# Kernel optimization log

Hardware: AMD Instinct MI355X
Metric: run time of the kernel (lower is better)

Reference implementation:

```python
import jax, jax.numpy as jnp
import numpy as np

B, D, F, FH = 8, 16, 16, 128
L = D * D
EPS = 1e-5


def _coords():
    i = np.arange(L, dtype=np.float64)
    c0 = ((i + 1) / D - D / 2) / (D / 2)
    c1 = ((i + 1) % D - D / 2) / (D / 2)
    return jnp.asarray(np.stack([c0, c1], axis=1), dtype=jnp.float32)  # (L, 2)


def setup_inputs() -> dict:
    key = jax.random.key(0)
    ks = jax.random.split(key, 16)
    s = 0.05
    fin = F + 2
    inp = {
        "x": jax.random.normal(ks[0], (B, F, D, D), jnp.float32),
        # g_fc1 weight split into the x_i half (first f+2 cols) and x_j half
        "W1a": jax.random.normal(ks[1], (fin, FH), jnp.float32) * s,
        "W1b": jax.random.normal(ks[2], (fin, FH), jnp.float32) * s,
        "b1": jnp.zeros((FH,), jnp.float32),
        "g1_gamma": jnp.ones((FH,), jnp.float32), "g1_beta": jnp.zeros((FH,), jnp.float32),
        "W2": jax.random.normal(ks[3], (FH, FH), jnp.float32) * s, "b2": jnp.zeros((FH,), jnp.float32),
        "g2_gamma": jnp.ones((FH,), jnp.float32), "g2_beta": jnp.zeros((FH,), jnp.float32),
        "W3": jax.random.normal(ks[4], (FH, FH), jnp.float32) * s, "b3": jnp.zeros((FH,), jnp.float32),
        "g3_gamma": jnp.ones((FH,), jnp.float32), "g3_beta": jnp.zeros((FH,), jnp.float32),
        "Wagg": jax.random.normal(ks[5], (L,), jnp.float32) * s, "bagg": jnp.zeros((), jnp.float32),
        "Wf": jax.random.normal(ks[6], (FH, FH), jnp.float32) * s, "bf": jnp.zeros((FH,), jnp.float32),
        "f_gamma": jnp.ones((FH,), jnp.float32), "f_beta": jnp.zeros((FH,), jnp.float32),
        "Wo2": jax.random.normal(ks[7], (FH, FH), jnp.float32) * s, "bo2": jnp.zeros((FH,), jnp.float32),
        "o2_gamma": jnp.ones((FH,), jnp.float32), "o2_beta": jnp.zeros((FH,), jnp.float32),
        "Wo3": jax.random.normal(ks[8], (FH, F), jnp.float32) * s, "bo3": jnp.zeros((F,), jnp.float32),
        "coord": _coords(),
    }
    return inp


def _bn(h, gamma, beta):
    # torch BatchNorm1d (training mode) applied over channel dim = last axis here;
    # stats over (batch, length), biased variance.
    mu = jnp.mean(h, axis=(0, 1))
    var = jnp.mean((h - mu) ** 2, axis=(0, 1))
    return gamma * (h - mu) * jax.lax.rsqrt(var + EPS) + beta


def reference(x, W1a, W1b, b1, g1_gamma, g1_beta, W2, b2, g2_gamma, g2_beta,
              W3, b3, g3_gamma, g3_beta, Wagg, bagg, Wf, bf, f_gamma, f_beta,
              Wo2, bo2, o2_gamma, o2_beta, Wo3, bo3, coord):
    b, f, d = x.shape[0], x.shape[1], x.shape[2]
    l = d * d
    x_flat = x.reshape(b, f, l).transpose(0, 2, 1)                     # (b, L, f)
    x_flat = jnp.concatenate([x_flat, jnp.broadcast_to(coord, (b, l, 2))], axis=2)  # (b, L, f+2)
    # g_fc1 on cat([x_i, x_j]): x_i varies along pair-dim2 (index l), x_j along dim1 (index k)
    hi = x_flat @ W1a                                                  # (b, L, FH)
    hj = x_flat @ W1b                                                  # (b, L, FH)
    h = hi[:, None, :, :] + hj[:, :, None, :] + b1                     # (b, L, L, FH)
    h = h.reshape(b, l * l, -1)
    h = jax.nn.relu(_bn(h, g1_gamma, g1_beta))
    h = jax.nn.relu(_bn(h @ W2 + b2, g2_gamma, g2_beta))
    h = jax.nn.relu(_bn(h @ W3 + b3, g3_gamma, g3_beta))
    x_g = h.reshape(b, l, l, -1)                                       # (b, k, l, FH)
    # affine_aggregate: Linear(L -> 1) over the l (dim2) axis after permute
    x_agg = jnp.einsum('bklf,l->bkf', x_g, Wagg) + bagg                # (b, L, FH)
    x_f = jax.nn.relu(_bn(x_agg @ Wf + bf, f_gamma, f_beta))
    xo = jax.nn.relu(_bn(x_f @ Wo2 + bo2, o2_gamma, o2_beta))
    out = xo @ Wo3 + bo3                                               # (b, L, f)
    return out.reshape(b, d, d, f).transpose(0, 3, 1, 2)               # (b, f, d, d)
```

## Files before the change

kernel.cpp:

```cpp
#include <hip/hip_runtime.h>
#include <hip/hip_bf16.h>

typedef __bf16 bf16x8 __attribute__((ext_vector_type(8)));
typedef float  f32x4  __attribute__((ext_vector_type(4)));

static constexpr size_t HI_OFF  = 0;
static constexpr size_t HJ_OFF  = HI_OFF + (1u << 20);
static constexpr size_t Z_OFF   = HJ_OFF + (1u << 20);
static constexpr size_t PS_OFF  = Z_OFF + (size_t)524288 * 128 * 2;
static constexpr size_t PQ_OFF  = PS_OFF + (size_t)4096 * 128 * 4;
static constexpr size_t S1I_OFF = PQ_OFF + (size_t)4096 * 128 * 4;
static constexpr size_t S2I_OFF = S1I_OFF + 4096;
static constexpr size_t S1J_OFF = S2I_OFF + 4096;
static constexpr size_t S2J_OFF = S1J_OFF + 4096;
static constexpr size_t A1_OFF  = S2J_OFF + 4096;
static constexpr size_t D1_OFF  = A1_OFF + 512;
static constexpr size_t A2_OFF  = D1_OFF + 512;
static constexpr size_t C2_OFF  = A2_OFF + 512;
static constexpr size_t A3_OFF  = C2_OFF + 512;
static constexpr size_t C3_OFF  = A3_OFF + 512;
static constexpr size_t AF_OFF  = C3_OFF + 512;
static constexpr size_t CF_OFF  = AF_OFF + 512;
static constexpr size_t AO_OFF  = CF_OFF + 512;
static constexpr size_t CO_OFF  = AO_OFF + 512;
static constexpr size_t W2T_OFF = CO_OFF + 512;
static constexpr size_t W3T_OFF = W2T_OFF + 32768;
static constexpr size_t XAGG_OFF = W3T_OFF + 32768;
static constexpr size_t Y1_OFF  = XAGG_OFF + (1u << 20);
static constexpr size_t Y2_OFF  = Y1_OFF + (1u << 20);
static constexpr size_t TPS_OFF = Y2_OFF + (1u << 20);
static constexpr size_t TPQ_OFF = TPS_OFF + 65536;

__global__ void build_h(const float* __restrict__ x, const float* __restrict__ coord,
                        const float* __restrict__ W1a, const float* __restrict__ W1b,
                        float* __restrict__ hi, float* __restrict__ hj)
{
    __shared__ float xr[18];
    int bl = blockIdx.x;
    int b = bl >> 8, l = bl & 255;
    int t = threadIdx.x;
    if (t < 18)
        xr[t] = (t < 16) ? x[((size_t)b * 16 + t) * 256 + l] : coord[l * 2 + (t - 16)];
    __syncthreads();
    float ai = 0.f, aj = 0.f;
#pragma unroll
    for (int c = 0; c < 18; ++c) {
        float xv = xr[c];
        ai += xv * W1a[c * 128 + t];
        aj += xv * W1b[c * 128 + t];
    }
    hi[(size_t)bl * 128 + t] = ai;
    hj[(size_t)bl * 128 + t] = aj;
}

__global__ void stats1(const float* __restrict__ hi, const float* __restrict__ hj,
                       float* __restrict__ S1i, float* __restrict__ S2i,
                       float* __restrict__ S1j, float* __restrict__ S2j)
{
    int b = blockIdx.x, f = threadIdx.x;
    float s1i = 0, s2i = 0, s1j = 0, s2j = 0;
    for (int l = 0; l < 256; ++l) {
        float vi = hi[((size_t)b * 256 + l) * 128 + f];
        float vj = hj[((size_t)b * 256 + l) * 128 + f];
        s1i += vi; s2i += vi * vi;
        s1j += vj; s2j += vj * vj;
    }
    S1i[b * 128 + f] = s1i; S2i[b * 128 + f] = s2i;
    S1j[b * 128 + f] = s1j; S2j[b * 128 + f] = s2j;
}

__global__ void bn1_finalize(const float* __restrict__ S1i, const float* __restrict__ S2i,
                             const float* __restrict__ S1j, const float* __restrict__ S2j,
                             const float* __restrict__ g, const float* __restrict__ be,
                             float* __restrict__ a1, float* __restrict__ d1,
                             const float* __restrict__ W2, const float* __restrict__ W3,
                             __bf16* __restrict__ W2t, __bf16* __restrict__ W3t)
{
    int f = threadIdx.x;
    float s1i = 0, s2i = 0, s1j = 0, s2j = 0;
    float mib[8], mjb[8];
#pragma unroll
    for (int b = 0; b < 8; ++b) {
        float x1 = S1i[b * 128 + f]; s1i += x1; mib[b] = x1 * (1.f / 256.f);
        s2i += S2i[b * 128 + f];
        float x2 = S1j[b * 128 + f]; s1j += x2; mjb[b] = x2 * (1.f / 256.f);
        s2j += S2j[b * 128 + f];
    }
    const float invN = 1.f / 2048.f;
    float mi = s1i * invN, mj = s1j * invN;
    float vu = s2i * invN - mi * mi;
    float vv = s2j * invN - mj * mj;
    float cr = 0.f;
#pragma unroll
    for (int b = 0; b < 8; ++b) cr += (mib[b] - mi) * (mjb[b] - mj);
    cr *= (1.f / 8.f);
    float var = vu + vv + 2.f * cr;
    float av = g[f] * rsqrtf(var + 1e-5f);
    a1[f] = av;
    d1[f] = be[f] - av * (mi + mj);
    for (int k = 0; k < 128; ++k) {
        W2t[f * 128 + k] = (__bf16)W2[k * 128 + f];
        W3t[f * 128 + k] = (__bf16)W3[k * 128 + f];
    }
}

__global__ __launch_bounds__(256) void pair_gemm1(
    const float* __restrict__ hi, const float* __restrict__ hj,
    const float* __restrict__ a1, const float* __restrict__ d1,
    const __bf16* __restrict__ W2t,
    __bf16* __restrict__ Z, float* __restrict__ ps, float* __restrict__ pq)
{
    __shared__ __align__(16) char hA[32768];
    __shared__ __align__(16) char wB[32768];
    __shared__ float red[1024];

    int blk = blockIdx.x;
    int half = blk & 1;
    int bk = blk >> 1;
    int b = bk >> 8;
    int t = threadIdx.x;
    int lane = t & 63;
    int wave = t >> 6;
    int fc = (t & 15) * 8;
    int rg = t >> 4;

    float a1v[8], qv[8];
    const float* hjrow = hj + (size_t)bk * 128 + fc;
    const float* d1p = d1 + fc;
    const float* a1p = a1 + fc;
#pragma unroll
    for (int j = 0; j < 8; ++j) { a1v[j] = a1p[j]; qv[j] = a1v[j] * hjrow[j] + d1p[j]; }

    const float* hib = hi + ((size_t)b * 256 + half * 128) * 128;
#pragma unroll
    for (int rr = 0; rr < 128; rr += 16) {
        int row = rr + rg;
        const float* src = hib + row * 128 + fc;
        bf16x8 v;
#pragma unroll
        for (int j = 0; j < 8; ++j) {
            float h = fmaxf(a1v[j] * src[j] + qv[j], 0.f);
            v[j] = (__bf16)h;
        }
        int byte = (row * 256 + fc * 2) ^ ((row & 7) << 4);
        *reinterpret_cast<bf16x8*>(hA + byte) = v;
        bf16x8 w = *reinterpret_cast<const bf16x8*>(W2t + row * 128 + fc);
        *reinterpret_cast<bf16x8*>(wB + byte) = w;
    }
    __syncthreads();

    f32x4 acc[2][8] = {};
    int arow0 = wave * 32 + (lane & 15);
    int kg = (lane >> 4) * 8;
#pragma unroll
    for (int kk = 0; kk < 128; kk += 32) {
        bf16x8 af[2], bfr[8];
#pragma unroll
        for (int m = 0; m < 2; ++m) {
            int row = arow0 + m * 16;
            int byte = (row * 256 + (kk + kg) * 2) ^ ((row & 7) << 4);
            af[m] = *reinterpret_cast<const bf16x8*>(hA + byte);
        }
#pragma unroll
        for (int n = 0; n < 8; ++n) {
            int col = n * 16 + (lane & 15);
            int byte = (col * 256 + (kk + kg) * 2) ^ ((col & 7) << 4);
            bfr[n] = *reinterpret_cast<const bf16x8*>(wB + byte);
        }
#pragma unroll
        for (int m = 0; m < 2; ++m)
#pragma unroll
            for (int n = 0; n < 8; ++n)
                acc[m][n] = __builtin_amdgcn_mfma_f32_16x16x32_bf16(af[m], bfr[n], acc[m][n], 0, 0, 0);
    }

    __bf16* zb = Z + ((size_t)bk * 256 + half * 128) * 128;
    float s[8] = {}, q[8] = {};
    int r0 = (lane >> 4) * 4;
    int cl = lane & 15;
#pragma unroll
    for (int m = 0; m < 2; ++m)
#pragma unroll
        for (int n = 0; n < 8; ++n)
#pragma unroll
            for (int r = 0; r < 4; ++r) {
                float v = acc[m][n][r];
                int row = wave * 32 + m * 16 + r0 + r;
                zb[row * 128 + n * 16 + cl] = (__bf16)v;
                s[n] += v; q[n] += v * v;
            }
#pragma unroll
    for (int n = 0; n < 8; ++n) {
        s[n] += __shfl_xor(s[n], 16); s[n] += __shfl_xor(s[n], 32);
        q[n] += __shfl_xor(q[n], 16); q[n] += __shfl_xor(q[n], 32);
    }
    if (lane < 16) {
#pragma unroll
        for (int n = 0; n < 8; ++n) {
            red[wave * 256 + n * 16 + cl] = s[n];
            red[wave * 256 + 128 + n * 16 + cl] = q[n];
        }
    }
    __syncthreads();
    {
        int f = t & 127, which = t >> 7;
        float a = red[0 * 256 + which * 128 + f] + red[1 * 256 + which * 128 + f]
                + red[2 * 256 + which * 128 + f] + red[3 * 256 + which * 128 + f];
        if (which == 0) ps[(size_t)blk * 128 + f] = a;
        else            pq[(size_t)blk * 128 + f] = a;
    }
}

__global__ __launch_bounds__(256) void pair_gemm2(
    __bf16* __restrict__ Z,
    const float* __restrict__ a2, const float* __restrict__ c2,
    const __bf16* __restrict__ W3t,
    float* __restrict__ ps, float* __restrict__ pq)
{
    __shared__ __align__(16) char hA[32768];
    __shared__ __align__(16) char wB[32768];
    __shared__ float red[1024];

    int blk = blockIdx.x;
    int half = blk & 1;
    int bk = blk >> 1;
    int t = threadIdx.x;
    int lane = t & 63;
    int wave = t >> 6;
    int fc = (t & 15) * 8;
    int rg = t >> 4;

    float a2v[8], c2v[8];
#pragma unroll
    for (int j = 0; j < 8; ++j) { a2v[j] = a2[fc + j]; c2v[j] = c2[fc + j]; }

    __bf16* zbase = Z + ((size_t)bk * 256 + half * 128) * 128;
#pragma unroll
    for (int rr = 0; rr < 128; rr += 16) {
        int row = rr + rg;
        bf16x8 zv = *reinterpret_cast<const bf16x8*>(zbase + row * 128 + fc);
        bf16x8 v;
#pragma unroll
        for (int j = 0; j < 8; ++j) {
            float h = fmaxf(a2v[j] * (float)zv[j] + c2v[j], 0.f);
            v[j] = (__bf16)h;
        }
        int byte = (row * 256 + fc * 2) ^ ((row & 7) << 4);
        *reinterpret_cast<bf16x8*>(hA + byte) = v;
        bf16x8 w = *reinterpret_cast<const bf16x8*>(W3t + row * 128 + fc);
        *reinterpret_cast<bf16x8*>(wB + byte) = w;
    }
    __syncthreads();

    f32x4 acc[2][8] = {};
    int arow0 = wave * 32 + (lane & 15);
    int kg = (lane >> 4) * 8;
#pragma unroll
    for (int kk = 0; kk < 128; kk += 32) {
        bf16x8 af[2], bfr[8];
#pragma unroll
        for (int m = 0; m < 2; ++m) {
            int row = arow0 + m * 16;
            int byte = (row * 256 + (kk + kg) * 2) ^ ((row & 7) << 4);
            af[m] = *reinterpret_cast<const bf16x8*>(hA + byte);
        }
#pragma unroll
        for (int n = 0; n < 8; ++n) {
            int col = n * 16 + (lane & 15);
            int byte = (col * 256 + (kk + kg) * 2) ^ ((col & 7) << 4);
            bfr[n] = *reinterpret_cast<const bf16x8*>(wB + byte);
        }
#pragma unroll
        for (int m = 0; m < 2; ++m)
#pragma unroll
            for (int n = 0; n < 8; ++n)
                acc[m][n] = __builtin_amdgcn_mfma_f32_16x16x32_bf16(af[m], bfr[n], acc[m][n], 0, 0, 0);
    }

    float s[8] = {}, q[8] = {};
    int r0 = (lane >> 4) * 4;
    int cl = lane & 15;
#pragma unroll
    for (int m = 0; m < 2; ++m)
#pragma unroll
        for (int n = 0; n < 8; ++n)
#pragma unroll
            for (int r = 0; r < 4; ++r) {
                float v = acc[m][n][r];
                int row = wave * 32 + m * 16 + r0 + r;
                zbase[row * 128 + n * 16 + cl] = (__bf16)v;
                s[n] += v; q[n] += v * v;
            }
#pragma unroll
    for (int n = 0; n < 8; ++n) {
        s[n] += __shfl_xor(s[n], 16); s[n] += __shfl_xor(s[n], 32);
        q[n] += __shfl_xor(q[n], 16); q[n] += __shfl_xor(q[n], 32);
    }
    if (lane < 16) {
#pragma unroll
        for (int n = 0; n < 8; ++n) {
            red[wave * 256 + n * 16 + cl] = s[n];
            red[wave * 256 + 128 + n * 16 + cl] = q[n];
        }
    }
    __syncthreads();
    {
        int f = t & 127, which = t >> 7;
        float a = red[0 * 256 + which * 128 + f] + red[1 * 256 + which * 128 + f]
                + red[2 * 256 + which * 128 + f] + red[3 * 256 + which * 128 + f];
        if (which == 0) ps[(size_t)blk * 128 + f] = a;
        else            pq[(size_t)blk * 128 + f] = a;
    }
}

__global__ void finalize_bn(const float* __restrict__ ps, const float* __restrict__ pq,
                            int nblk, float inv_count,
                            const float* __restrict__ gamma, const float* __restrict__ beta,
                            float* __restrict__ a, float* __restrict__ c)
{
    __shared__ float rs[256], rq[256];
    int f = blockIdx.x, t = threadIdx.x;
    float s = 0, q = 0;
    for (int i = t; i < nblk; i += 256) {
        s += ps[(size_t)i * 128 + f];
        q += pq[(size_t)i * 128 + f];
    }
    rs[t] = s; rq[t] = q;
    __syncthreads();
    for (int st = 128; st > 0; st >>= 1) {
        if (t < st) { rs[t] += rs[t + st]; rq[t] += rq[t + st]; }
        __syncthreads();
    }
    if (t == 0) {
        float mean = rs[0] * inv_count;
        float var = rq[0] * inv_count - mean * mean;
        float av = gamma[f] * rsqrtf(var + 1e-5f);
        a[f] = av;
        c[f] = beta[f] - av * mean;
    }
}

__global__ void aggregate(const __bf16* __restrict__ Z,
                          const float* __restrict__ a3, const float* __restrict__ c3,
                          const float* __restrict__ Wagg, const float* __restrict__ bagg,
                          float* __restrict__ xagg)
{
    int bk = blockIdx.x;
    int f = threadIdx.x;
    const __bf16* zb = Z + (size_t)bk * 256 * 128 + f;
    float av = a3[f], cv = c3[f];
    float acc = 0.f;
#pragma unroll 4
    for (int l = 0; l < 256; ++l) {
        float v = (float)zb[(size_t)l * 128];
        v = fmaxf(av * v + cv, 0.f);
        acc += v * Wagg[l];
    }
    xagg[(size_t)bk * 128 + f] = acc + bagg[0];
}

__global__ void tail_gemm(const float* __restrict__ X,
                          const float* __restrict__ aIn, const float* __restrict__ cIn, int relu_in,
                          const float* __restrict__ W, const float* __restrict__ bias,
                          float* __restrict__ Y, float* __restrict__ ps, float* __restrict__ pq)
{
    __shared__ float xs[2048];
    __shared__ float rsum[256];
    int blk = blockIdx.x, t = threadIdx.x;
    for (int i = t; i < 2048; i += 256) {
        float v = X[(size_t)blk * 2048 + i];
        if (relu_in) { int f = i & 127; v = fmaxf(aIn[f] * v + cIn[f], 0.f); }
        xs[i] = v;
    }
    __syncthreads();
    int col = t & 127, hf = t >> 7;
    float bv = bias[col];
    float acc[8];
#pragma unroll
    for (int r = 0; r < 8; ++r) acc[r] = bv;
    for (int k = 0; k < 128; ++k) {
        float w = W[k * 128 + col];
#pragma unroll
        for (int r = 0; r < 8; ++r) acc[r] += xs[(hf * 8 + r) * 128 + k] * w;
    }
    float s = 0, q = 0;
#pragma unroll
    for (int r = 0; r < 8; ++r) {
        Y[((size_t)blk * 16 + hf * 8 + r) * 128 + col] = acc[r];
        s += acc[r]; q += acc[r] * acc[r];
    }
    rsum[t] = s; __syncthreads();
    if (hf == 0) ps[(size_t)blk * 128 + col] = rsum[col] + rsum[128 + col];
    __syncthreads();
    rsum[t] = q; __syncthreads();
    if (hf == 0) pq[(size_t)blk * 128 + col] = rsum[col] + rsum[128 + col];
}

__global__ void tail_out(const float* __restrict__ Y2,
                         const float* __restrict__ ao, const float* __restrict__ co,
                         const float* __restrict__ Wo3, const float* __restrict__ bo3,
                         float* __restrict__ out)
{
    __shared__ float xs[2048];
    int blk = blockIdx.x, t = threadIdx.x;
    for (int i = t; i < 2048; i += 256) {
        int f = i & 127;
        xs[i] = fmaxf(ao[f] * Y2[(size_t)blk * 2048 + i] + co[f], 0.f);
    }
    __syncthreads();
    int col = t & 15, r = t >> 4;
    float acc = bo3[col];
    for (int k = 0; k < 128; ++k) acc += xs[r * 128 + k] * Wo3[k * 16 + col];
    int grow = blk * 16 + r;
    int b = grow >> 8, l = grow & 255;
    out[((size_t)b * 16 + col) * 256 + l] = acc;
}

extern "C" void kernel_launch(void* const* d_in, const int* in_sizes, int n_in,
                              void* d_out, int out_size, void* d_ws, size_t ws_size,
                              hipStream_t stream)
{
    const float* x     = (const float*)d_in[0];
    const float* W1a   = (const float*)d_in[1];
    const float* W1b   = (const float*)d_in[2];
    const float* g1g   = (const float*)d_in[4];
    const float* g1b   = (const float*)d_in[5];
    const float* W2    = (const float*)d_in[6];
    const float* g2g   = (const float*)d_in[8];
    const float* g2b   = (const float*)d_in[9];
    const float* W3    = (const float*)d_in[10];
    const float* g3g   = (const float*)d_in[12];
    const float* g3b   = (const float*)d_in[13];
    const float* Wagg  = (const float*)d_in[14];
    const float* bagg  = (const float*)d_in[15];
    const float* Wf    = (const float*)d_in[16];
    const float* bf_   = (const float*)d_in[17];
    const float* fg    = (const float*)d_in[18];
    const float* fb    = (const float*)d_in[19];
    const float* Wo2   = (const float*)d_in[20];
    const float* bo2   = (const float*)d_in[21];
    const float* og    = (const float*)d_in[22];
    const float* ob    = (const float*)d_in[23];
    const float* Wo3   = (const float*)d_in[24];
    const float* bo3   = (const float*)d_in[25];
    const float* coord = (const float*)d_in[26];

    char* ws = (char*)d_ws;
    float*  HI   = (float*)(ws + HI_OFF);
    float*  HJ   = (float*)(ws + HJ_OFF);
    __bf16* Z    = (__bf16*)(ws + Z_OFF);
    float*  PS   = (float*)(ws + PS_OFF);
    float*  PQ   = (float*)(ws + PQ_OFF);
    float*  S1I  = (float*)(ws + S1I_OFF);
    float*  S2I  = (float*)(ws + S2I_OFF);
    float*  S1J  = (float*)(ws + S1J_OFF);
    float*  S2J  = (float*)(ws + S2J_OFF);
    float*  A1   = (float*)(ws + A1_OFF);
    float*  D1   = (float*)(ws + D1_OFF);
    float*  A2   = (float*)(ws + A2_OFF);
    float*  C2   = (float*)(ws + C2_OFF);
    float*  A3   = (float*)(ws + A3_OFF);
    float*  C3   = (float*)(ws + C3_OFF);
    float*  AF   = (float*)(ws + AF_OFF);
    float*  CF   = (float*)(ws + CF_OFF);
    float*  AO   = (float*)(ws + AO_OFF);
    float*  CO   = (float*)(ws + CO_OFF);
    __bf16* W2T  = (__bf16*)(ws + W2T_OFF);
    __bf16* W3T  = (__bf16*)(ws + W3T_OFF);
    float*  XAGG = (float*)(ws + XAGG_OFF);
    float*  Y1   = (float*)(ws + Y1_OFF);
    float*  Y2   = (float*)(ws + Y2_OFF);
    float*  TPS  = (float*)(ws + TPS_OFF);
    float*  TPQ  = (float*)(ws + TPQ_OFF);

    build_h<<<2048, 128, 0, stream>>>(x, coord, W1a, W1b, HI, HJ);
    stats1<<<8, 128, 0, stream>>>(HI, HJ, S1I, S2I, S1J, S2J);
    bn1_finalize<<<1, 128, 0, stream>>>(S1I, S2I, S1J, S2J, g1g, g1b, A1, D1, W2, W3, W2T, W3T);

    pair_gemm1<<<4096, 256, 0, stream>>>(HI, HJ, A1, D1, W2T, Z, PS, PQ);
    finalize_bn<<<128, 256, 0, stream>>>(PS, PQ, 4096, 1.f / 524288.f, g2g, g2b, A2, C2);

    pair_gemm2<<<4096, 256, 0, stream>>>(Z, A2, C2, W3T, PS, PQ);
    finalize_bn<<<128, 256, 0, stream>>>(PS, PQ, 4096, 1.f / 524288.f, g3g, g3b, A3, C3);

    aggregate<<<2048, 128, 0, stream>>>(Z, A3, C3, Wagg, bagg, XAGG);

    tail_gemm<<<128, 256, 0, stream>>>(XAGG, A1, D1, 0, Wf, bf_, Y1, TPS, TPQ);
    finalize_bn<<<128, 256, 0, stream>>>(TPS, TPQ, 128, 1.f / 2048.f, fg, fb, AF, CF);

    tail_gemm<<<128, 256, 0, stream>>>(Y1, AF, CF, 1, Wo2, bo2, Y2, TPS, TPQ);
    finalize_bn<<<128, 256, 0, stream>>>(TPS, TPQ, 128, 1.f / 2048.f, og, ob, AO, CO);

    tail_out<<<128, 256, 0, stream>>>(Y2, AO, CO, Wo3, bo3, (float*)d_out);

    (void)in_sizes; (void)n_in; (void)out_size; (void)ws_size;
}
```

Baseline: 217.1 us.

## Recompute layer-3 GEMM fused with aggregation instead of writing Z back

```diff
diff --git a/kernel.cpp b/kernel.cpp
--- a/kernel.cpp
+++ b/kernel.cpp
@@ -2,18 +2,22 @@
 #include <hip/hip_bf16.h>
 
 typedef __bf16 bf16x8 __attribute__((ext_vector_type(8)));
+typedef __bf16 bf16x4 __attribute__((ext_vector_type(4)));
 typedef float  f32x4  __attribute__((ext_vector_type(4)));
 
+static constexpr size_t MB = 1u << 20;
 static constexpr size_t HI_OFF  = 0;
-static constexpr size_t HJ_OFF  = HI_OFF + (1u << 20);
-static constexpr size_t Z_OFF   = HJ_OFF + (1u << 20);
+static constexpr size_t HJ_OFF  = HI_OFF + MB;
+static constexpr size_t HIS_OFF = HJ_OFF + MB;
+static constexpr size_t QV_OFF  = HIS_OFF + MB;
+static constexpr size_t Z_OFF   = QV_OFF + MB;
 static constexpr size_t PS_OFF  = Z_OFF + (size_t)524288 * 128 * 2;
 static constexpr size_t PQ_OFF  = PS_OFF + (size_t)4096 * 128 * 4;
 static constexpr size_t S1I_OFF = PQ_OFF + (size_t)4096 * 128 * 4;
-static constexpr size_t S2I_OFF = S1I_OFF + 4096;
-static constexpr size_t S1J_OFF = S2I_OFF + 4096;
-static constexpr size_t S2J_OFF = S1J_OFF + 4096;
-static constexpr size_t A1_OFF  = S2J_OFF + 4096;
+static constexpr size_t S2I_OFF = S1I_OFF + 32768;
+static constexpr size_t S1J_OFF = S2I_OFF + 32768;
+static constexpr size_t S2J_OFF = S1J_OFF + 32768;
+static constexpr size_t A1_OFF  = S2J_OFF + 32768;
 static constexpr size_t D1_OFF  = A1_OFF + 512;
 static constexpr size_t A2_OFF  = D1_OFF + 512;
 static constexpr size_t C2_OFF  = A2_OFF + 512;
@@ -26,9 +30,9 @@
 static constexpr size_t W2T_OFF = CO_OFF + 512;
 static constexpr size_t W3T_OFF = W2T_OFF + 32768;
 static constexpr size_t XAGG_OFF = W3T_OFF + 32768;
-static constexpr size_t Y1_OFF  = XAGG_OFF + (1u << 20);
-static constexpr size_t Y2_OFF  = Y1_OFF + (1u << 20);
-static constexpr size_t TPS_OFF = Y2_OFF + (1u << 20);
+static constexpr size_t Y1_OFF  = XAGG_OFF + MB;
+static constexpr size_t Y2_OFF  = Y1_OFF + MB;
+static constexpr size_t TPS_OFF = Y2_OFF + MB;
 static constexpr size_t TPQ_OFF = TPS_OFF + 65536;
 
 __global__ void build_h(const float* __restrict__ x, const float* __restrict__ coord,
@@ -57,34 +61,41 @@
                        float* __restrict__ S1i, float* __restrict__ S2i,
                        float* __restrict__ S1j, float* __restrict__ S2j)
 {
-    int b = blockIdx.x, f = threadIdx.x;
+    int g = blockIdx.x;
+    int b = g >> 3, lg = g & 7;
+    int f = threadIdx.x;
     float s1i = 0, s2i = 0, s1j = 0, s2j = 0;
-    for (int l = 0; l < 256; ++l) {
+#pragma unroll 4
+    for (int i = 0; i < 32; ++i) {
+        int l = lg * 32 + i;
         float vi = hi[((size_t)b * 256 + l) * 128 + f];
         float vj = hj[((size_t)b * 256 + l) * 128 + f];
         s1i += vi; s2i += vi * vi;
         s1j += vj; s2j += vj * vj;
     }
-    S1i[b * 128 + f] = s1i; S2i[b * 128 + f] = s2i;
-    S1j[b * 128 + f] = s1j; S2j[b * 128 + f] = s2j;
+    S1i[g * 128 + f] = s1i; S2i[g * 128 + f] = s2i;
+    S1j[g * 128 + f] = s1j; S2j[g * 128 + f] = s2j;
 }
 
 __global__ void bn1_finalize(const float* __restrict__ S1i, const float* __restrict__ S2i,
                              const float* __restrict__ S1j, const float* __restrict__ S2j,
                              const float* __restrict__ g, const float* __restrict__ be,
-                             float* __restrict__ a1, float* __restrict__ d1,
-                             const float* __restrict__ W2, const float* __restrict__ W3,
-                             __bf16* __restrict__ W2t, __bf16* __restrict__ W3t)
+                             float* __restrict__ a1, float* __restrict__ d1)
 {
     int f = threadIdx.x;
     float s1i = 0, s2i = 0, s1j = 0, s2j = 0;
     float mib[8], mjb[8];
 #pragma unroll
     for (int b = 0; b < 8; ++b) {
-        float x1 = S1i[b * 128 + f]; s1i += x1; mib[b] = x1 * (1.f / 256.f);
-        s2i += S2i[b * 128 + f];
-        float x2 = S1j[b * 128 + f]; s1j += x2; mjb[b] = x2 * (1.f / 256.f);
-        s2j += S2j[b * 128 + f];
+        float sb = 0, sbj = 0;
+#pragma unroll
+        for (int lg = 0; lg < 8; ++lg) {
+            int gg = b * 8 + lg;
+            sb  += S1i[gg * 128 + f]; s2i += S2i[gg * 128 + f];
+            sbj += S1j[gg * 128 + f]; s2j += S2j[gg * 128 + f];
+        }
+        mib[b] = sb * (1.f / 256.f); mjb[b] = sbj * (1.f / 256.f);
+        s1i += sb; s1j += sbj;
     }
     const float invN = 1.f / 2048.f;
     float mi = s1i * invN, mj = s1j * invN;
@@ -98,219 +109,294 @@
     float av = g[f] * rsqrtf(var + 1e-5f);
     a1[f] = av;
     d1[f] = be[f] - av * (mi + mj);
-    for (int k = 0; k < 128; ++k) {
-        W2t[f * 128 + k] = (__bf16)W2[k * 128 + f];
-        W3t[f * 128 + k] = (__bf16)W3[k * 128 + f];
-    }
-}
-
-__global__ __launch_bounds__(256) void pair_gemm1(
-    const float* __restrict__ hi, const float* __restrict__ hj,
-    const float* __restrict__ a1, const float* __restrict__ d1,
-    const __bf16* __restrict__ W2t,
-    __bf16* __restrict__ Z, float* __restrict__ ps, float* __restrict__ pq)
-{
-    __shared__ __align__(16) char hA[32768];
-    __shared__ __align__(16) char wB[32768];
-    __shared__ float red[1024];
+}
+
+__global__ void transpose_w(const float* __restrict__ W2, const float* __restrict__ W3,
+                            __bf16* __restrict__ W2t, __bf16* __restrict__ W3t)
+{
+    int f = blockIdx.x, k = threadIdx.x;
+    W2t[f * 128 + k] = (__bf16)W2[k * 128 + f];
+    W3t[f * 128 + k] = (__bf16)W3[k * 128 + f];
+}
+
+__global__ void scale_h(const float* __restrict__ hi, const float* __restrict__ hj,
+                        const float* __restrict__ a1, const float* __restrict__ d1,
+                        float* __restrict__ his, float* __restrict__ qv)
+{
+    int bl = blockIdx.x, f = threadIdx.x;
+    float a = a1[f];
+    his[(size_t)bl * 128 + f] = a * hi[(size_t)bl * 128 + f];
+    qv[(size_t)bl * 128 + f]  = a * hj[(size_t)bl * 128 + f] + d1[f];
+}
+
+__global__ __launch_bounds__(256) void pair_stage1(
+    const float* __restrict__ HIS, const float* __restrict__ QV,
+    const __bf16* __restrict__ W2t, __bf16* __restrict__ Z,
+    float* __restrict__ ps, float* __restrict__ pq)
+{
+    __shared__ __align__(16) char wlds[32768];
+    __shared__ float red[2][4][128];
 
     int blk = blockIdx.x;
-    int half = blk & 1;
-    int bk = blk >> 1;
-    int b = bk >> 8;
-    int t = threadIdx.x;
-    int lane = t & 63;
-    int wave = t >> 6;
-    int fc = (t & 15) * 8;
-    int rg = t >> 4;
-
-    float a1v[8], qv[8];
-    const float* hjrow = hj + (size_t)bk * 128 + fc;
-    const float* d1p = d1 + fc;
-    const float* a1p = a1 + fc;
-#pragma unroll
-    for (int j = 0; j < 8; ++j) { a1v[j] = a1p[j]; qv[j] = a1v[j] * hjrow[j] + d1p[j]; }
-
-    const float* hib = hi + ((size_t)b * 256 + half * 128) * 128;
-#pragma unroll
-    for (int rr = 0; rr < 128; rr += 16) {
-        int row = rr + rg;
-        const float* src = hib + row * 128 + fc;
-        bf16x8 v;
-#pragma unroll
-        for (int j = 0; j < 8; ++j) {
-            float h = fmaxf(a1v[j] * src[j] + qv[j], 0.f);
-            v[j] = (__bf16)h;
-        }
-        int byte = (row * 256 + fc * 2) ^ ((row & 7) << 4);
-        *reinterpret_cast<bf16x8*>(hA + byte) = v;
-        bf16x8 w = *reinterpret_cast<const bf16x8*>(W2t + row * 128 + fc);
-        *reinterpret_cast<bf16x8*>(wB + byte) = w;
-    }
-    __syncthreads();
+    int bk = blk >> 1, half = blk & 1;
+    int b  = bk >> 8;
+    int t = threadIdx.x, lane = t & 63, wave = t >> 6;
+    int cl = lane & 15, kg = lane >> 4;
+
+    {
+        int fcs = t & 15, rs = t >> 4;
+#pragma unroll
+        for (int i = 0; i < 8; ++i) {
+            int row = rs + i * 16;
+            bf16x8 w = *reinterpret_cast<const bf16x8*>(W2t + row * 128 + fcs * 8);
+            int byte = row * 256 + ((fcs * 16) ^ ((row & 7) << 4));
+            *reinterpret_cast<bf16x8*>(wlds + byte) = w;
+        }
+    }
+    __syncthreads();
+
+    int lrow0 = half * 128 + wave * 32;
+    size_t zrow0 = (size_t)bk * 256 + lrow0;
+    const float* qvp = QV + (size_t)bk * 128;
 
     f32x4 acc[2][8] = {};
-    int arow0 = wave * 32 + (lane & 15);
-    int kg = (lane >> 4) * 8;
-#pragma unroll
-    for (int kk = 0; kk < 128; kk += 32) {
-        bf16x8 af[2], bfr[8];
+#pragma unroll
+    for (int kk = 0; kk < 4; ++kk) {
+        int ko = kk * 32 + kg * 8;
+        f32x4 q0 = *reinterpret_cast<const f32x4*>(qvp + ko);
+        f32x4 q1 = *reinterpret_cast<const f32x4*>(qvp + ko + 4);
+        bf16x8 Af[2];
 #pragma unroll
         for (int m = 0; m < 2; ++m) {
-            int row = arow0 + m * 16;
-            int byte = (row * 256 + (kk + kg) * 2) ^ ((row & 7) << 4);
-            af[m] = *reinterpret_cast<const bf16x8*>(hA + byte);
+            const float* hp = HIS + ((size_t)(b * 256 + lrow0 + m * 16 + cl)) * 128 + ko;
+            f32x4 h0 = *reinterpret_cast<const f32x4*>(hp);
+            f32x4 h1 = *reinterpret_cast<const f32x4*>(hp + 4);
+#pragma unroll
+            for (int j = 0; j < 4; ++j) {
+                Af[m][j]     = (__bf16)fmaxf(h0[j] + q0[j], 0.f);
+                Af[m][j + 4] = (__bf16)fmaxf(h1[j] + q1[j], 0.f);
+            }
         }
 #pragma unroll
         for (int n = 0; n < 8; ++n) {
-            int col = n * 16 + (lane & 15);
-            int byte = (col * 256 + (kk + kg) * 2) ^ ((col & 7) << 4);
-            bfr[n] = *reinterpret_cast<const bf16x8*>(wB + byte);
-        }
-#pragma unroll
-        for (int m = 0; m < 2; ++m)
-#pragma unroll
-            for (int n = 0; n < 8; ++n)
-                acc[m][n] = __builtin_amdgcn_mfma_f32_16x16x32_bf16(af[m], bfr[n], acc[m][n], 0, 0, 0);
-    }
-
-    __bf16* zb = Z + ((size_t)bk * 256 + half * 128) * 128;
-    float s[8] = {}, q[8] = {};
-    int r0 = (lane >> 4) * 4;
-    int cl = lane & 15;
-#pragma unroll
-    for (int m = 0; m < 2; ++m)
-#pragma unroll
-        for (int n = 0; n < 8; ++n)
+            int r = n * 16 + cl;
+            int byte = r * 256 + (((kk * 4 + kg) * 16) ^ ((cl & 7) << 4));
+            bf16x8 Bf = *reinterpret_cast<const bf16x8*>(wlds + byte);
+#pragma unroll
+            for (int m = 0; m < 2; ++m)
+                acc[m][n] = __builtin_amdgcn_mfma_f32_16x16x32_bf16(Bf, Af[m], acc[m][n], 0, 0, 0);
+        }
+    }
+
+#pragma unroll
+    for (int n = 0; n < 8; ++n) {
+        float sv[4], q2[4];
+#pragma unroll
+        for (int m = 0; m < 2; ++m) {
+            bf16x4 pv;
 #pragma unroll
             for (int r = 0; r < 4; ++r) {
                 float v = acc[m][n][r];
-                int row = wave * 32 + m * 16 + r0 + r;
-                zb[row * 128 + n * 16 + cl] = (__bf16)v;
-                s[n] += v; q[n] += v * v;
-            }
-#pragma unroll
-    for (int n = 0; n < 8; ++n) {
-        s[n] += __shfl_xor(s[n], 16); s[n] += __shfl_xor(s[n], 32);
-        q[n] += __shfl_xor(q[n], 16); q[n] += __shfl_xor(q[n], 32);
-    }
-    if (lane < 16) {
-#pragma unroll
-        for (int n = 0; n < 8; ++n) {
-            red[wave * 256 + n * 16 + cl] = s[n];
-            red[wave * 256 + 128 + n * 16 + cl] = q[n];
-        }
-    }
-    __syncthreads();
-    {
-        int f = t & 127, which = t >> 7;
-        float a = red[0 * 256 + which * 128 + f] + red[1 * 256 + which * 128 + f]
-                + red[2 * 256 + which * 128 + f] + red[3 * 256 + which * 128 + f];
-        if (which == 0) ps[(size_t)blk * 128 + f] = a;
-        else            pq[(size_t)blk * 128 + f] = a;
-    }
-}
-
-__global__ __launch_bounds__(256) void pair_gemm2(
-    __bf16* __restrict__ Z,
+                pv[r] = (__bf16)v;
+                if (m == 0) { sv[r] = v;  q2[r] = v * v; }
+                else        { sv[r] += v; q2[r] += v * v; }
+            }
+            *reinterpret_cast<bf16x4*>(Z + (zrow0 + m * 16 + cl) * 128 + n * 16 + kg * 4) = pv;
+        }
+#pragma unroll
+        for (int r = 0; r < 4; ++r) {
+            sv[r] += __shfl_xor(sv[r], 1); sv[r] += __shfl_xor(sv[r], 2);
+            sv[r] += __shfl_xor(sv[r], 4); sv[r] += __shfl_xor(sv[r], 8);
+            q2[r] += __shfl_xor(q2[r], 1); q2[r] += __shfl_xor(q2[r], 2);
+            q2[r] += __shfl_xor(q2[r], 4); q2[r] += __shfl_xor(q2[r], 8);
+        }
+        if (cl == 0) {
+#pragma unroll
+            for (int r = 0; r < 4; ++r) {
+                red[0][wave][n * 16 + kg * 4 + r] = sv[r];
+                red[1][wave][n * 16 + kg * 4 + r] = q2[r];
+            }
+        }
+    }
+    __syncthreads();
+    if (t < 128) {
+        ps[(size_t)blk * 128 + t] = red[0][0][t] + red[0][1][t] + red[0][2][t] + red[0][3][t];
+        pq[(size_t)blk * 128 + t] = red[1][0][t] + red[1][1][t] + red[1][2][t] + red[1][3][t];
+    }
+}
+
+__global__ __launch_bounds__(256) void pair_stage2(
+    const __bf16* __restrict__ Z,
     const float* __restrict__ a2, const float* __restrict__ c2,
     const __bf16* __restrict__ W3t,
     float* __restrict__ ps, float* __restrict__ pq)
 {
-    __shared__ __align__(16) char hA[32768];
-    __shared__ __align__(16) char wB[32768];
-    __shared__ float red[1024];
+    __shared__ __align__(16) char wlds[32768];
+    __shared__ float red[2][4][128];
 
     int blk = blockIdx.x;
-    int half = blk & 1;
-    int bk = blk >> 1;
-    int t = threadIdx.x;
-    int lane = t & 63;
-    int wave = t >> 6;
-    int fc = (t & 15) * 8;
-    int rg = t >> 4;
-
-    float a2v[8], c2v[8];
-#pragma unroll
-    for (int j = 0; j < 8; ++j) { a2v[j] = a2[fc + j]; c2v[j] = c2[fc + j]; }
-
-    __bf16* zbase = Z + ((size_t)bk * 256 + half * 128) * 128;
-#pragma unroll
-    for (int rr = 0; rr < 128; rr += 16) {
-        int row = rr + rg;
-        bf16x8 zv = *reinterpret_cast<const bf16x8*>(zbase + row * 128 + fc);
-        bf16x8 v;
-#pragma unroll
-        for (int j = 0; j < 8; ++j) {
-            float h = fmaxf(a2v[j] * (float)zv[j] + c2v[j], 0.f);
-            v[j] = (__bf16)h;
-        }
-        int byte = (row * 256 + fc * 2) ^ ((row & 7) << 4);
-        *reinterpret_cast<bf16x8*>(hA + byte) = v;
-        bf16x8 w = *reinterpret_cast<const bf16x8*>(W3t + row * 128 + fc);
-        *reinterpret_cast<bf16x8*>(wB + byte) = w;
-    }
-    __syncthreads();
+    int bk = blk >> 1, half = blk & 1;
+    int t = threadIdx.x, lane = t & 63, wave = t >> 6;
+    int cl = lane & 15, kg = lane >> 4;
+
+    {
+        int fcs = t & 15, rs = t >> 4;
+#pragma unroll
+        for (int i = 0; i < 8; ++i) {
+            int row = rs + i * 16;
+            bf16x8 w = *reinterpret_cast<const bf16x8*>(W3t + row * 128 + fcs * 8);
+            int byte = row * 256 + ((fcs * 16) ^ ((row & 7) << 4));
+            *reinterpret_cast<bf16x8*>(wlds + byte) = w;
+        }
+    }
+    __syncthreads();
+
+    size_t row0 = (size_t)bk * 256 + half * 128 + wave * 32;
 
     f32x4 acc[2][8] = {};
-    int arow0 = wave * 32 + (lane & 15);
-    int kg = (lane >> 4) * 8;
-#pragma unroll
-    for (int kk = 0; kk < 128; kk += 32) {
-        bf16x8 af[2], bfr[8];
+#pragma unroll
+    for (int kk = 0; kk < 4; ++kk) {
+        int ko = kk * 32 + kg * 8;
+        f32x4 a2l = *reinterpret_cast<const f32x4*>(a2 + ko);
+        f32x4 a2h = *reinterpret_cast<const f32x4*>(a2 + ko + 4);
+        f32x4 c2l = *reinterpret_cast<const f32x4*>(c2 + ko);
+        f32x4 c2h = *reinterpret_cast<const f32x4*>(c2 + ko + 4);
+        bf16x8 Af[2];
 #pragma unroll
         for (int m = 0; m < 2; ++m) {
-            int row = arow0 + m * 16;
-            int byte = (row * 256 + (kk + kg) * 2) ^ ((row & 7) << 4);
-            af[m] = *reinterpret_cast<const bf16x8*>(hA + byte);
+            bf16x8 zv = *reinterpret_cast<const bf16x8*>(Z + (row0 + m * 16 + cl) * 128 + ko);
+#pragma unroll
+            for (int j = 0; j < 4; ++j) {
+                Af[m][j]     = (__bf16)fmaxf(a2l[j] * (float)zv[j] + c2l[j], 0.f);
+                Af[m][j + 4] = (__bf16)fmaxf(a2h[j] * (float)zv[j + 4] + c2h[j], 0.f);
+            }
         }
 #pragma unroll
         for (int n = 0; n < 8; ++n) {
-            int col = n * 16 + (lane & 15);
-            int byte = (col * 256 + (kk + kg) * 2) ^ ((col & 7) << 4);
-            bfr[n] = *reinterpret_cast<const bf16x8*>(wB + byte);
-        }
-#pragma unroll
-        for (int m = 0; m < 2; ++m)
-#pragma unroll
-            for (int n = 0; n < 8; ++n)
-                acc[m][n] = __builtin_amdgcn_mfma_f32_16x16x32_bf16(af[m], bfr[n], acc[m][n], 0, 0, 0);
-    }
-
-    float s[8] = {}, q[8] = {};
-    int r0 = (lane >> 4) * 4;
-    int cl = lane & 15;
-#pragma unroll
-    for (int m = 0; m < 2; ++m)
-#pragma unroll
-        for (int n = 0; n < 8; ++n)
+            int r = n * 16 + cl;
+            int byte = r * 256 + (((kk * 4 + kg) * 16) ^ ((cl & 7) << 4));
+            bf16x8 Bf = *reinterpret_cast<const bf16x8*>(wlds + byte);
+#pragma unroll
+            for (int m = 0; m < 2; ++m)
+                acc[m][n] = __builtin_amdgcn_mfma_f32_16x16x32_bf16(Bf, Af[m], acc[m][n], 0, 0, 0);
+        }
+    }
+
+#pragma unroll
+    for (int n = 0; n < 8; ++n) {
+        float sv[4], q2[4];
+#pragma unroll
+        for (int r = 0; r < 4; ++r) {
+            float v0 = acc[0][n][r], v1 = acc[1][n][r];
+            sv[r] = v0 + v1; q2[r] = v0 * v0 + v1 * v1;
+            sv[r] += __shfl_xor(sv[r], 1); sv[r] += __shfl_xor(sv[r], 2);
+            sv[r] += __shfl_xor(sv[r], 4); sv[r] += __shfl_xor(sv[r], 8);
+            q2[r] += __shfl_xor(q2[r], 1); q2[r] += __shfl_xor(q2[r], 2);
+            q2[r] += __shfl_xor(q2[r], 4); q2[r] += __shfl_xor(q2[r], 8);
+        }
+        if (cl == 0) {
 #pragma unroll
             for (int r = 0; r < 4; ++r) {
-                float v = acc[m][n][r];
-                int row = wave * 32 + m * 16 + r0 + r;
-                zbase[row * 128 + n * 16 + cl] = (__bf16)v;
-                s[n] += v; q[n] += v * v;
-            }
+                red[0][wave][n * 16 + kg * 4 + r] = sv[r];
+                red[1][wave][n * 16 + kg * 4 + r] = q2[r];
+            }
+        }
+    }
+    __syncthreads();
+    if (t < 128) {
+        ps[(size_t)blk * 128 + t] = red[0][0][t] + red[0][1][t] + red[0][2][t] + red[0][3][t];
+        pq[(size_t)blk * 128 + t] = red[1][0][t] + red[1][1][t] + red[1][2][t] + red[1][3][t];
+    }
+}
+
+__global__ __launch_bounds__(256) void pair_stage3(
+    const __bf16* __restrict__ Z,
+    const float* __restrict__ a2, const float* __restrict__ c2,
+    const __bf16* __restrict__ W3t,
+    const float* __restrict__ a3, const float* __restrict__ c3,
+    const float* __restrict__ Wagg, const float* __restrict__ bagg,
+    float* __restrict__ xagg)
+{
+    __shared__ __align__(16) char wlds[32768];
+    __shared__ float red[4][128];
+
+    int bk = blockIdx.x;
+    int t = threadIdx.x, lane = t & 63, wave = t >> 6;
+    int cl = lane & 15, kg = lane >> 4;
+
+    {
+        int fcs = t & 15, rs = t >> 4;
+#pragma unroll
+        for (int i = 0; i < 8; ++i) {
+            int row = rs + i * 16;
+            bf16x8 w = *reinterpret_cast<const bf16x8*>(W3t + row * 128 + fcs * 8);
+            int byte = row * 256 + ((fcs * 16) ^ ((row & 7) << 4));
+            *reinterpret_cast<bf16x8*>(wlds + byte) = w;
+        }
+    }
+    __syncthreads();
+
+    float ag[8][4] = {};
+
+#pragma unroll
+    for (int it = 0; it < 2; ++it) {
+        size_t row0 = (size_t)bk * 256 + wave * 64 + it * 32;
+        f32x4 acc[2][8] = {};
+#pragma unroll
+        for (int kk = 0; kk < 4; ++kk) {
+            int ko = kk * 32 + kg * 8;
+            f32x4 a2l = *reinterpret_cast<const f32x4*>(a2 + ko);
+            f32x4 a2h = *reinterpret_cast<const f32x4*>(a2 + ko + 4);
+            f32x4 c2l = *reinterpret_cast<const f32x4*>(c2 + ko);
+            f32x4 c2h = *reinterpret_cast<const f32x4*>(c2 + ko + 4);
+            bf16x8 Af[2];
+#pragma unroll
+            for (int m = 0; m < 2; ++m) {
+                bf16x8 zv = *reinterpret_cast<const bf16x8*>(Z + (row0 + m * 16 + cl) * 128 + ko);
+#pragma unroll
+                for (int j = 0; j < 4; ++j) {
+                    Af[m][j]     = (__bf16)fmaxf(a2l[j] * (float)zv[j] + c2l[j], 0.f);
+                    Af[m][j + 4] = (__bf16)fmaxf(a2h[j] * (float)zv[j + 4] + c2h[j], 0.f);
+                }
+            }
+#pragma unroll
+            for (int n = 0; n < 8; ++n) {
+                int r = n * 16 + cl;
+                int byte = r * 256 + (((kk * 4 + kg) * 16) ^ ((cl & 7) << 4));
+                bf16x8 Bf = *reinterpret_cast<const bf16x8*>(wlds + byte);
+#pragma unroll
+                for (int m = 0; m < 2; ++m)
+                    acc[m][n] = __builtin_amdgcn_mfma_f32_16x16x32_bf16(Bf, Af[m], acc[m][n], 0, 0, 0);
+            }
+        }
+        int lb = wave * 64 + it * 32;
+        float w0 = Wagg[lb + cl];
+        float w1 = Wagg[lb + 16 + cl];
+#pragma unroll
+        for (int n = 0; n < 8; ++n) {
+            f32x4 a3v = *reinterpret_cast<const f32x4*>(a3 + n * 16 + kg * 4);
+            f32x4 c3v = *reinterpret_cast<const f32x4*>(c3 + n * 16 + kg * 4);
+#pragma unroll
+            for (int r = 0; r < 4; ++r) {
+                ag[n][r] += w0 * fmaxf(a3v[r] * acc[0][n][r] + c3v[r], 0.f)
+                          + w1 * fmaxf(a3v[r] * acc[1][n][r] + c3v[r], 0.f);
+            }
+        }
+    }
+
 #pragma unroll
     for (int n = 0; n < 8; ++n) {
-        s[n] += __shfl_xor(s[n], 16); s[n] += __shfl_xor(s[n], 32);
-        q[n] += __shfl_xor(q[n], 16); q[n] += __shfl_xor(q[n], 32);
-    }
-    if (lane < 16) {
-#pragma unroll
-        for (int n = 0; n < 8; ++n) {
-            red[wave * 256 + n * 16 + cl] = s[n];
-            red[wave * 256 + 128 + n * 16 + cl] = q[n];
-        }
-    }
-    __syncthreads();
-    {
-        int f = t & 127, which = t >> 7;
-        float a = red[0 * 256 + which * 128 + f] + red[1 * 256 + which * 128 + f]
-                + red[2 * 256 + which * 128 + f] + red[3 * 256 + which * 128 + f];
-        if (which == 0) ps[(size_t)blk * 128 + f] = a;
-        else            pq[(size_t)blk * 128 + f] = a;
-    }
+#pragma unroll
+        for (int r = 0; r < 4; ++r) {
+            float v = ag[n][r];
+            v += __shfl_xor(v, 1); v += __shfl_xor(v, 2);
+            v += __shfl_xor(v, 4); v += __shfl_xor(v, 8);
+            if (cl == 0) red[wave][n * 16 + kg * 4 + r] = v;
+        }
+    }
+    __syncthreads();
+    if (t < 128)
+        xagg[(size_t)bk * 128 + t] = red[0][t] + red[1][t] + red[2][t] + red[3][t] + bagg[0];
 }
 
 __global__ void finalize_bn(const float* __restrict__ ps, const float* __restrict__ pq,
@@ -338,25 +424,6 @@
         a[f] = av;
         c[f] = beta[f] - av * mean;
     }
-}
-
-__global__ void aggregate(const __bf16* __restrict__ Z,
-                          const float* __restrict__ a3, const float* __restrict__ c3,
-                          const float* __restrict__ Wagg, const float* __restrict__ bagg,
-                          float* __restrict__ xagg)
-{
-    int bk = blockIdx.x;
-    int f = threadIdx.x;
-    const __bf16* zb = Z + (size_t)bk * 256 * 128 + f;
-    float av = a3[f], cv = c3[f];
-    float acc = 0.f;
-#pragma unroll 4
-    for (int l = 0; l < 256; ++l) {
-        float v = (float)zb[(size_t)l * 128];
-        v = fmaxf(av * v + cv, 0.f);
-        acc += v * Wagg[l];
-    }
-    xagg[(size_t)bk * 128 + f] = acc + bagg[0];
 }
 
 __global__ void tail_gemm(const float* __restrict__ X,
@@ -448,6 +515,8 @@
     char* ws = (char*)d_ws;
     float*  HI   = (float*)(ws + HI_OFF);
     float*  HJ   = (float*)(ws + HJ_OFF);
+    float*  HIS  = (float*)(ws + HIS_OFF);
+    float*  QV   = (float*)(ws + QV_OFF);
     __bf16* Z    = (__bf16*)(ws + Z_OFF);
     float*  PS   = (float*)(ws + PS_OFF);
     float*  PQ   = (float*)(ws + PQ_OFF);
@@ -474,16 +543,18 @@
     float*  TPQ  = (float*)(ws + TPQ_OFF);
 
     build_h<<<2048, 128, 0, stream>>>(x, coord, W1a, W1b, HI, HJ);
-    stats1<<<8, 128, 0, stream>>>(HI, HJ, S1I, S2I, S1J, S2J);
-    bn1_finalize<<<1, 128, 0, stream>>>(S1I, S2I, S1J, S2J, g1g, g1b, A1, D1, W2, W3, W2T, W3T);
-
-    pair_gemm1<<<4096, 256, 0, stream>>>(HI, HJ, A1, D1, W2T, Z, PS, PQ);
+    stats1<<<64, 128, 0, stream>>>(HI, HJ, S1I, S2I, S1J, S2J);
+    bn1_finalize<<<1, 128, 0, stream>>>(S1I, S2I, S1J, S2J, g1g, g1b, A1, D1);
+    transpose_w<<<128, 128, 0, stream>>>(W2, W3, W2T, W3T);
+    scale_h<<<2048, 128, 0, stream>>>(HI, HJ, A1, D1, HIS, QV);
+
+    pair_stage1<<<4096, 256, 0, stream>>>(HIS, QV, W2T, Z, PS, PQ);
     finalize_bn<<<128, 256, 0, stream>>>(PS, PQ, 4096, 1.f / 524288.f, g2g, g2b, A2, C2);
 
-    pair_gemm2<<<4096, 256, 0, stream>>>(Z, A2, C2, W3T, PS, PQ);
+    pair_stage2<<<4096, 256, 0, stream>>>(Z, A2, C2, W3T, PS, PQ);
     finalize_bn<<<128, 256, 0, stream>>>(PS, PQ, 4096, 1.f / 524288.f, g3g, g3b, A3, C3);
 
-    aggregate<<<2048, 128, 0, stream>>>(Z, A3, C3, Wagg, bagg, XAGG);
+    pair_stage3<<<2048, 256, 0, stream>>>(Z, A2, C2, W3T, A3, C3, Wagg, bagg, XAGG);
 
     tail_gemm<<<128, 256, 0, stream>>>(XAGG, A1, D1, 0, Wf, bf_, Y1, TPS, TPQ);
     finalize_bn<<<128, 256, 0, stream>>>(TPS, TPQ, 128, 1.f / 2048.f, fg, fb, AF, CF);
```

Result: slower. 312.7 us (+44.1%).
